# Kernel optimization log

Hardware: AMD Instinct MI355X
Metric: run time of the kernel (lower is better)

The kernel has to match this reference:

```python
import jax, jax.numpy as jnp
import numpy as np

N = 50000      # nodes
E = 800000     # edges (avg degree 16)
IN_DIM = 128
H = 4          # attention heads
D = 32         # hidden dim per head
NEG_SLOPE = 0.2


def setup_inputs() -> dict:
    key = jax.random.key(0)
    ks = jax.random.split(key, 9)
    x = jax.random.normal(ks[0], (N, IN_DIM), dtype=jnp.float32)
    src = jax.random.randint(ks[1], (E,), 0, N, dtype=jnp.int64)
    dst = jax.random.randint(ks[2], (E,), 0, N, dtype=jnp.int64)
    # layer 0: IN_DIM -> H*D ; layer 1: H*D -> H*D
    s0 = 1.0 / np.sqrt(IN_DIM)
    s1 = 1.0 / np.sqrt(H * D)
    W1 = jax.random.normal(ks[3], (H * D, IN_DIM), dtype=jnp.float32) * s0
    al1 = jax.random.normal(ks[4], (1, H, D), dtype=jnp.float32) * s1
    ar1 = jax.random.normal(ks[5], (1, H, D), dtype=jnp.float32) * s1
    W2 = jax.random.normal(ks[6], (H * D, H * D), dtype=jnp.float32) * s1
    al2 = jax.random.normal(ks[7], (1, H, D), dtype=jnp.float32) * s1
    ar2 = jax.random.normal(ks[8], (1, H, D), dtype=jnp.float32) * s1
    return {"x": x, "src": src, "dst": dst, "W1": W1, "al1": al1, "ar1": ar1,
            "W2": W2, "al2": al2, "ar2": ar2}


def gat_conv(h, src, dst, W, al, ar):
    """DGL-style GATConv. h: [N, F_in] -> [N, H, D], with ELU activation."""
    feat = (h @ W.T).reshape(N, H, D)                 # [N,H,D]
    el = jnp.sum(feat * al, axis=-1)                  # [N,H] a_l . Wh
    er = jnp.sum(feat * ar, axis=-1)                  # [N,H] a_r . Wh
    e = jax.nn.leaky_relu(el[src] + er[dst], NEG_SLOPE)  # [E,H]
    # numerically stable edge softmax over incoming edges of each dst node
    m = jax.ops.segment_max(e, dst, num_segments=N)   # [N,H]
    ee = jnp.exp(e - m[dst])                          # [E,H]
    denom = jax.ops.segment_sum(ee, dst, num_segments=N)  # [N,H]
    alpha = ee / denom[dst]                           # [E,H]
    msg = feat[src] * alpha[..., None]                # [E,H,D]
    out = jax.ops.segment_sum(msg, dst, num_segments=N)   # [N,H,D]
    return jax.nn.elu(out)


def reference(x, src, dst, W1, al1, ar1, W2, al2, ar2):
    h = gat_conv(x, src, dst, W1, al1, ar1).reshape(N, H * D)  # flatten(1)
    h = gat_conv(h, src, dst, W2, al2, ar2)                    # [N,H,D]
    return jnp.mean(h, axis=1)                                 # [N,D]
```

## Files before the change

### kernel.cpp

```cpp
#include <hip/hip_runtime.h>
#include <cmath>
#include <type_traits>

#define HEADS 4
#define FDIM 128
#define NEG 0.2f
#define NBUCK 8
#define CSHIFT 7
#define CMASK 127

typedef __attribute__((ext_vector_type(8))) __bf16 bf16x8;
typedef __attribute__((ext_vector_type(8))) _Float16 h16x8;
typedef __attribute__((ext_vector_type(4))) float f32x4;

__global__ __launch_bounds__(256) void prep_kernel(
    const float* __restrict__ W1, const float* __restrict__ al1,
    const float* __restrict__ ar1,
    const float* __restrict__ W2, const float* __restrict__ al2,
    const float* __restrict__ ar2,
    __bf16* __restrict__ wf1, __bf16* __restrict__ wext1,
    _Float16* __restrict__ wf2, _Float16* __restrict__ wext2)
{
    const int b = blockIdx.x, tid = threadIdx.x;
    if (b < 256) {
        int idx = (b & 127) * 256 + tid;
        int j = idx & 7;
        int r = idx >> 3;
        int c = r & 15; r >>= 4;
        int t = r & 7;  r >>= 3;
        int kq = r & 15;
        int hl = r >> 4;
        if (b < 128) {
            float v = W1[(t * 16 + c) * 128 + kq * 8 + j];
            __bf16 hi = (__bf16)v;
            wf1[idx] = (hl == 0) ? hi : (__bf16)(v - (float)hi);
        } else {
            float v = W2[(t * 16 + c) * 128 + kq * 8 + j];
            _Float16 hi = (_Float16)v;
            wf2[idx] = (hl == 0) ? hi : (_Float16)(v - (float)hi);
        }
    } else {
        const float* W  = (b == 256) ? W1 : W2;
        const float* al = (b == 256) ? al1 : al2;
        const float* ar = (b == 256) ? ar1 : ar2;
        __shared__ float val[1024];
        #pragma unroll
        for (int ch = 0; ch < 4; ++ch) {
            int idx = ch * 256 + tid;
            int c = idx >> 7, k = idx & 127;
            int h = c & 3;
            const float* a = (c < 4) ? al : ar;
            float s = 0.f;
            for (int d = 0; d < 32; ++d)
                s += a[h * 32 + d] * W[(h * 32 + d) * 128 + k];
            val[c * 128 + k] = s;
        }
        __syncthreads();
        #pragma unroll
        for (int ch = 0; ch < 16; ++ch) {
            int idx = tid * 16 + ch;
            int j = idx & 7;
            int r = idx >> 3;
            int c = r & 15; r >>= 4;
            int kq = r & 15;
            int hl = r >> 4;
            float v = (c < 8) ? val[c * 128 + kq * 8 + j] : 0.f;
            if (b == 256) {
                __bf16 hi = (__bf16)v;
                wext1[idx] = (hl == 0) ? hi : (__bf16)(v - (float)hi);
            } else {
                _Float16 hi = (_Float16)v;
                wext2[idx] = (hl == 0) ? hi : (_Float16)(v - (float)hi);
            }
        }
    }
}

__device__ __forceinline__ void gemm_body_f32(
    const float* __restrict__ X, const bf16x8* __restrict__ wf,
    const bf16x8* __restrict__ wext, _Float16* __restrict__ featH,
    float* __restrict__ el, float* __restrict__ er,
    int nnodes, int tile0, int tend, int stride, bf16x8* lw)
{
    const int tid = threadIdx.x;
    const int wave = tid >> 6, lane = tid & 63;
    const int l15 = lane & 15, quad = lane >> 4;

    int tile = tile0;
    float xr[32], xn[32];

    auto loadX = [&](int tl, float* dst) {
        int nodeA = tl * 64 + wave * 16 + l15;
        bool v = nodeA < nnodes;
        const float4* xp = (const float4*)(X + (size_t)nodeA * 128);
        #pragma unroll
        for (int ks = 0; ks < 4; ++ks) {
            float4 a = v ? xp[ks * 8 + quad * 2]     : make_float4(0.f, 0.f, 0.f, 0.f);
            float4 b = v ? xp[ks * 8 + quad * 2 + 1] : make_float4(0.f, 0.f, 0.f, 0.f);
            dst[ks * 8 + 0] = a.x; dst[ks * 8 + 1] = a.y;
            dst[ks * 8 + 2] = a.z; dst[ks * 8 + 3] = a.w;
            dst[ks * 8 + 4] = b.x; dst[ks * 8 + 5] = b.y;
            dst[ks * 8 + 6] = b.z; dst[ks * 8 + 7] = b.w;
        }
    };

    loadX(tile, xr);
    for (int i = tid; i < 2048; i += 256) lw[i] = wf[i];
    __syncthreads();

    while (true) {
        int next = tile + stride;
        if (next < tend) loadX(next, xn);

        f32x4 acc[9];
        #pragma unroll
        for (int t = 0; t < 9; ++t) acc[t] = (f32x4){0.f, 0.f, 0.f, 0.f};

        #pragma unroll
        for (int ks = 0; ks < 4; ++ks) {
            bf16x8 ahi, alo;
            #pragma unroll
            for (int j = 0; j < 8; ++j) {
                float xv = xr[ks * 8 + j];
                __bf16 h = (__bf16)xv;
                ahi[j] = h;
                alo[j] = (__bf16)(xv - (float)h);
            }
            const int kq = ks * 4 + quad;

            {
                bf16x8 bh = wext[(kq) * 16 + l15];
                bf16x8 bl = wext[(16 + kq) * 16 + l15];
                acc[8] = __builtin_amdgcn_mfma_f32_16x16x32_bf16(ahi, bh, acc[8], 0, 0, 0);
                acc[8] = __builtin_amdgcn_mfma_f32_16x16x32_bf16(alo, bh, acc[8], 0, 0, 0);
                acc[8] = __builtin_amdgcn_mfma_f32_16x16x32_bf16(ahi, bl, acc[8], 0, 0, 0);
            }
            #pragma unroll
            for (int t = 0; t < 8; ++t) {
                bf16x8 bh = lw[(kq * 8 + t) * 16 + l15];
                bf16x8 bl = wf[2048 + (kq * 8 + t) * 16 + l15];
                acc[t] = __builtin_amdgcn_mfma_f32_16x16x32_bf16(ahi, bh, acc[t], 0, 0, 0);
                acc[t] = __builtin_amdgcn_mfma_f32_16x16x32_bf16(alo, bh, acc[t], 0, 0, 0);
                acc[t] = __builtin_amdgcn_mfma_f32_16x16x32_bf16(ahi, bl, acc[t], 0, 0, 0);
            }
        }

        const int nodeC = tile * 64 + wave * 16 + quad * 4;
        #pragma unroll
        for (int r = 0; r < 4; ++r) {
            int gn = nodeC + r;
            if (gn < nnodes) {
                #pragma unroll
                for (int t = 0; t < 8; ++t)
                    featH[(size_t)gn * 128 + t * 16 + l15] = (_Float16)acc[t][r];
            }
        }
        if (l15 < 8) {
            #pragma unroll
            for (int r = 0; r < 4; ++r) {
                int gn = nodeC + r;
                if (gn < nnodes) {
                    if (l15 < 4) el[gn * HEADS + l15] = acc[8][r];
                    else         er[gn * HEADS + (l15 - 4)] = acc[8][r];
                }
            }
        }

        if (next >= tend) break;
        #pragma unroll
        for (int i = 0; i < 32; ++i) xr[i] = xn[i];
        tile = next;
    }
}

__device__ __forceinline__ void coarse_hist_body(
    const int* __restrict__ dst, int* __restrict__ histmat,
    int nedges, int nblk, int nbkt, int eb, int* chist)
{
    const int tid = threadIdx.x;
    for (int i = tid; i < nbkt; i += 256) chist[i] = 0;
    __syncthreads();
    int i0 = eb * 2048 + tid * 8;
    if (i0 + 7 < nedges) {
        int4 d0 = *(const int4*)&dst[i0];
        int4 d1 = *(const int4*)&dst[i0 + 4];
        atomicAdd(&chist[d0.x >> CSHIFT], 1);
        atomicAdd(&chist[d0.y >> CSHIFT], 1);
        atomicAdd(&chist[d0.z >> CSHIFT], 1);
        atomicAdd(&chist[d0.w >> CSHIFT], 1);
        atomicAdd(&chist[d1.x >> CSHIFT], 1);
        atomicAdd(&chist[d1.y >> CSHIFT], 1);
        atomicAdd(&chist[d1.z >> CSHIFT], 1);
        atomicAdd(&chist[d1.w >> CSHIFT], 1);
    } else {
        for (int i = i0; i < nedges; ++i)
            atomicAdd(&chist[dst[i] >> CSHIFT], 1);
    }
    __syncthreads();
    for (int i = tid; i < nbkt; i += 256)
        histmat[i * nblk + eb] = chist[i];
}

__device__ __forceinline__ void coarse_scatter_body(
    const int* __restrict__ src, const int* __restrict__ dst,
    const int* __restrict__ histoff, int* __restrict__ tmp,
    int nedges, int nblk, int nbkt, int eb, int* chist)
{
    const int tid = threadIdx.x;
    for (int i = tid; i < nbkt; i += 256) chist[i] = 0;
    __syncthreads();
    int i0 = eb * 2048 + tid * 8;
    if (i0 + 7 < nedges) {
        int s[8], d[8];
        *(int4*)&s[0] = *(const int4*)&src[i0];
        *(int4*)&s[4] = *(const int4*)&src[i0 + 4];
        *(int4*)&d[0] = *(const int4*)&dst[i0];
        *(int4*)&d[4] = *(const int4*)&dst[i0 + 4];
        #pragma unroll
        for (int q = 0; q < 8; ++q) {
            int bkt = d[q] >> CSHIFT;
            int r = atomicAdd(&chist[bkt], 1);
            int pos = histoff[bkt * nblk + eb] + r;
            tmp[pos] = ((d[q] & CMASK) << 16) | s[q];
        }
    } else {
        for (int i = i0; i < nedges; ++i) {
            int s = src[i], d = dst[i];
            int bkt = d >> CSHIFT;
            int r = atomicAdd(&chist[bkt], 1);
            tmp[histoff[bkt * nblk + eb] + r] = ((d & CMASK) << 16) | s;
        }
    }
}

__global__ __launch_bounds__(256) void fused_gemm_chist(
    const float* __restrict__ X, const bf16x8* __restrict__ wf,
    const bf16x8* __restrict__ wext, _Float16* __restrict__ featH,
    float* __restrict__ el, float* __restrict__ er, int nnodes,
    int t0, int tend, int gemm_blocks,
    const int* __restrict__ dst, int* __restrict__ histmat,
    int nedges, int nblk, int nbkt)
{
    __shared__ bf16x8 lw[2048];
    __shared__ int chist[512];
    if ((int)blockIdx.x < gemm_blocks)
        gemm_body_f32(X, wf, wext, featH, el, er, nnodes,
                      t0 + blockIdx.x, tend, gemm_blocks, lw);
    else
        coarse_hist_body(dst, histmat, nedges, nblk, nbkt,
                         blockIdx.x - gemm_blocks, chist);
}

__global__ __launch_bounds__(256) void fused_gemm_cscatter(
    const float* __restrict__ X, const bf16x8* __restrict__ wf,
    const bf16x8* __restrict__ wext, _Float16* __restrict__ featH,
    float* __restrict__ el, float* __restrict__ er, int nnodes,
    int t0, int tend, int gemm_blocks,
    const int* __restrict__ src, const int* __restrict__ dst,
    const int* __restrict__ histoff, int* __restrict__ tmp,
    int nedges, int nblk, int nbkt)
{
    __shared__ bf16x8 lw[2048];
    __shared__ int chist[512];
    if ((int)blockIdx.x < gemm_blocks)
        gemm_body_f32(X, wf, wext, featH, el, er, nnodes,
                      t0 + blockIdx.x, tend, gemm_blocks, lw);
    else
        coarse_scatter_body(src, dst, histoff, tmp, nedges, nblk, nbkt,
                            blockIdx.x - gemm_blocks, chist);
}

__global__ __launch_bounds__(256) void fine_sort_kernel(
    const int* __restrict__ tmp, const int* __restrict__ histoff,
    int* __restrict__ csr_src, int* __restrict__ offsets,
    int nblk, int nbkt, int nb, int nedges, int shift)
{
    __shared__ int eds[4096];
    __shared__ int fh[1024];
    __shared__ int wsums[4];
    const int b = blockIdx.x, tid = threadIdx.x;
    const int lane = tid & 63, w = tid >> 6;

    const int base = histoff[b * nblk];
    const int endb = histoff[(b + 1) * nblk];
    int cnt = endb - base;
    if (cnt > 4096) cnt = 4096;

    #pragma unroll
    for (int i = 0; i < 4; ++i) fh[tid + i * 256] = 0;
    __syncthreads();

    for (int i = tid; i < cnt; i += 256) {
        int e = tmp[base + i];
        eds[i] = e;
        int fb = ((e >> 16) << 3) + ((e & 0xffff) >> shift);
        atomicAdd(&fh[fb], 1);
    }
    __syncthreads();

    int v0 = fh[tid * 4], v1 = fh[tid * 4 + 1], v2 = fh[tid * 4 + 2], v3 = fh[tid * 4 + 3];
    int s0 = v0, s1 = s0 + v1, s2 = s1 + v2, s3 = s2 + v3;
    int x = s3;
    #pragma unroll
    for (int off = 1; off < 64; off <<= 1) {
        int t = __shfl_up(x, off, 64);
        if (lane >= off) x += t;
    }
    if (lane == 63) wsums[w] = x;
    __syncthreads();
    int wbase = 0;
    #pragma unroll
    for (int k = 0; k < 4; ++k) if (k < w) wbase += wsums[k];
    const int tb = wbase + x - s3;

    int o0 = tb, o1 = tb + s0, o2 = tb + s1, o3 = tb + s2;
    fh[tid * 4]     = o0;
    fh[tid * 4 + 1] = o1;
    fh[tid * 4 + 2] = o2;
    fh[tid * 4 + 3] = o3;
    int g = b * 1024 + tid * 4;
    if (g < nb)     offsets[g]     = base + o0;
    if (g + 1 < nb) offsets[g + 1] = base + o1;
    if (g + 2 < nb) offsets[g + 2] = base + o2;
    if (g + 3 < nb) offsets[g + 3] = base + o3;
    __syncthreads();

    for (int i = tid; i < cnt; i += 256) {
        int e = eds[i];
        int fb = ((e >> 16) << 3) + ((e & 0xffff) >> shift);
        int p = atomicAdd(&fh[fb], 1);
        csr_src[base + p] = e & 0xffff;
    }
    if (b == 0 && tid == 0) offsets[nb] = nedges;
}

__global__ __launch_bounds__(256) void scan1_kernel(
    const int* __restrict__ counts, int* __restrict__ offsets,
    int* __restrict__ bsums, int n)
{
    __shared__ int wsums[4];
    const int tid = threadIdx.x, lane = tid & 63, w = tid >> 6;
    const int i = blockIdx.x * 1024 + tid * 4;

    int4 v = make_int4(0, 0, 0, 0);
    if (i + 3 < n) v = *(const int4*)&counts[i];
    else {
        if (i < n)     v.x = counts[i];
        if (i + 1 < n) v.y = counts[i + 1];
        if (i + 2 < n) v.z = counts[i + 2];
    }
    int s0 = v.x, s1 = s0 + v.y, s2 = s1 + v.z, s3 = s2 + v.w;

    int x = s3;
    #pragma unroll
    for (int off = 1; off < 64; off <<= 1) {
        int t = __shfl_up(x, off, 64);
        if (lane >= off) x += t;
    }
    if (lane == 63) wsums[w] = x;
    __syncthreads();
    int wbase = 0;
    #pragma unroll
    for (int k = 0; k < 4; ++k) if (k < w) wbase += wsums[k];

    int tbase = wbase + x - s3;
    if (i < n)     offsets[i]     = tbase;
    if (i + 1 < n) offsets[i + 1] = tbase + s0;
    if (i + 2 < n) offsets[i + 2] = tbase + s1;
    if (i + 3 < n) offsets[i + 3] = tbase + s2;
    if (tid == 255) bsums[blockIdx.x] = wbase + x;
}

__global__ __launch_bounds__(256) void scan23_kernel(
    int* __restrict__ offsets, const int* __restrict__ bsums, int n, int nedges)
{
    __shared__ int sbase;
    const int tid = threadIdx.x, b = blockIdx.x;
    if (tid < 64) {
        int s = 0;
        for (int i = tid; i < b; i += 64) s += bsums[i];
        #pragma unroll
        for (int off = 1; off < 64; off <<= 1) s += __shfl_xor(s, off, 64);
        if (tid == 0) sbase = s;
    }
    __syncthreads();
    const int base = sbase;
    const int i = b * 1024 + tid * 4;
    #pragma unroll
    for (int k = 0; k < 4; ++k)
        if (i + k < n) offsets[i + k] += base;
    if (b == 0 && tid == 0) offsets[n] = nedges;
}

__device__ __forceinline__ void agg_one_node(
    const h16x8* __restrict__ frow, const float* __restrict__ el,
    const int* __restrict__ csr_src, int beg, int end,
    int g, int u, int h, float ern, float* r)
{
    float a[8];
    #pragma unroll
    for (int p = 0; p < 8; ++p) a[p] = 0.f;
    float sw = 0.f;
    const int iters = (end - beg + 3) >> 2;

    int ja = beg + g;
    int jb = ja + 4;
    int jc = ja + 8;
    int jd = ja + 12;
    bool va = ja < end, vb = jb < end;
    int sa = va ? csr_src[ja] : 0;
    int sb = vb ? csr_src[jb] : 0;
    int sc = jc < end ? csr_src[jc] : 0;
    int sd = jd < end ? csr_src[jd] : 0;
    float qa = el[sa * HEADS + h];
    float qb = el[sb * HEADS + h];
    h16x8 fa = frow[(size_t)sa * 16 + u];
    h16x8 fb = frow[(size_t)sb * 16 + u];

    for (int it = 0; it < iters; ++it) {
        int je = jd + 4;
        int se = je < end ? csr_src[je] : 0;
        float qc = el[sc * HEADS + h];
        h16x8 fc = frow[(size_t)sc * 16 + u];

        float e = qa + ern;
        e = e > 0.f ? e : NEG * e;
        float w2 = va ? __expf(e) : 0.f;
        #pragma unroll
        for (int p = 0; p < 8; ++p) a[p] += w2 * (float)fa[p];
        sw += w2;

        ja = jb; va = vb;
        jb = jc; vb = jb < end;
        qa = qb; fa = fb;
        qb = qc; fb = fc;
        sc = sd; sd = se;
        jc = jd; jd = je;
    }

    #pragma unroll
    for (int p = 0; p < 8; ++p) {
        a[p] += __shfl_xor(a[p], 16, 64);
        a[p] += __shfl_xor(a[p], 32, 64);
    }
    sw += __shfl_xor(sw, 16, 64);
    sw += __shfl_xor(sw, 32, 64);

    float inv = sw > 0.f ? 1.f / sw : 0.f;
    #pragma unroll
    for (int p = 0; p < 8; ++p) {
        float t = a[p] * inv;
        r[p] = t > 0.f ? t : __expf(t) - 1.f;
    }
}

__global__ __launch_bounds__(256) void fused_agg1_gemm2(
    const _Float16* __restrict__ featH, const float* __restrict__ el,
    const float* __restrict__ er, const int* __restrict__ offsets,
    const int* __restrict__ csr_src,
    const h16x8* __restrict__ wf, const h16x8* __restrict__ wext,
    _Float16* __restrict__ featH2, float* __restrict__ el2,
    float* __restrict__ er2, int nnodes)
{
    __shared__ h16x8 lw[2048];
    __shared__ h16x8 xt[1024];
    const int tid = threadIdx.x;
    const int wave = tid >> 6, lane = tid & 63;
    const int l15 = lane & 15, quad = lane >> 4;
    const int g = lane >> 4, u = lane & 15, h = u >> 2;
    const int tile = blockIdx.x;

    for (int i = tid; i < 2048; i += 256) lw[i] = wf[i];

    const h16x8* frow = (const h16x8*)featH;

    for (int i = 0; i < 16; ++i) {
        int row = wave * 16 + i;
        int n = tile * 64 + row;
        int scol = u ^ (row & 15);
        if (n < nnodes) {
            int beg = offsets[n * NBUCK], end = offsets[n * NBUCK + NBUCK];
            float ern = er[n * HEADS + h];
            float r[8];
            agg_one_node(frow, el, csr_src, beg, end, g, u, h, ern, r);
            if (g == 0) {
                h16x8 o;
                #pragma unroll
                for (int p = 0; p < 8; ++p) o[p] = (_Float16)r[p];
                xt[row * 16 + scol] = o;
            }
        } else if (g == 0) {
            h16x8 z;
            #pragma unroll
            for (int p = 0; p < 8; ++p) z[p] = (_Float16)0.f;
            xt[row * 16 + scol] = z;
        }
    }
    __syncthreads();

    f32x4 acc[9];
    #pragma unroll
    for (int t = 0; t < 9; ++t) acc[t] = (f32x4){0.f, 0.f, 0.f, 0.f};

    #pragma unroll
    for (int ks = 0; ks < 4; ++ks) {
        const int kq = ks * 4 + quad;
        h16x8 a = xt[(wave * 16 + l15) * 16 + (kq ^ l15)];
        {
            h16x8 bh = wext[(kq) * 16 + l15];
            h16x8 bl = wext[(16 + kq) * 16 + l15];
            acc[8] = __builtin_amdgcn_mfma_f32_16x16x32_f16(a, bh, acc[8], 0, 0, 0);
            acc[8] = __builtin_amdgcn_mfma_f32_16x16x32_f16(a, bl, acc[8], 0, 0, 0);
        }
        #pragma unroll
        for (int t = 0; t < 8; ++t) {
            h16x8 bh = lw[(kq * 8 + t) * 16 + l15];
            h16x8 bl = wf[2048 + (kq * 8 + t) * 16 + l15];
            acc[t] = __builtin_amdgcn_mfma_f32_16x16x32_f16(a, bh, acc[t], 0, 0, 0);
            acc[t] = __builtin_amdgcn_mfma_f32_16x16x32_f16(a, bl, acc[t], 0, 0, 0);
        }
    }

    const int nodeC = tile * 64 + wave * 16 + quad * 4;
    #pragma unroll
    for (int r = 0; r < 4; ++r) {
        int gn = nodeC + r;
        if (gn < nnodes) {
            #pragma unroll
            for (int t = 0; t < 8; ++t)
                featH2[(size_t)gn * 128 + t * 16 + l15] = (_Float16)acc[t][r];
        }
    }
    if (l15 < 8) {
        #pragma unroll
        for (int r = 0; r < 4; ++r) {
            int gn = nodeC + r;
            if (gn < nnodes) {
                if (l15 < 4) el2[gn * HEADS + l15] = acc[8][r];
                else         er2[gn * HEADS + (l15 - 4)] = acc[8][r];
            }
        }
    }
}

__global__ __launch_bounds__(256) void aggregate_mean_kernel(
    const _Float16* __restrict__ featH, const float* __restrict__ el,
    const float* __restrict__ er, const int* __restrict__ offsets,
    const int* __restrict__ csr_src, float* __restrict__ outp, int nnodes)
{
    const int n = (blockIdx.x * 256 + threadIdx.x) >> 6;
    if (n >= nnodes) return;
    const int lane = threadIdx.x & 63;
    const int g = lane >> 4, u = lane & 15, h = u >> 2;
    const int beg = offsets[n * NBUCK], end = offsets[n * NBUCK + NBUCK];
    const float ern = er[n * HEADS + h];

    float r[8];
    agg_one_node((const h16x8*)featH, el, csr_src, beg, end, g, u, h, ern, r);

    #pragma unroll
    for (int p = 0; p < 8; ++p) {
        r[p] += __shfl_xor(r[p], 4, 64);
        r[p] += __shfl_xor(r[p], 8, 64);
    }
    if (g == 0 && u < 4) {
        float4* o4 = (float4*)(outp + (size_t)n * 32 + u * 8);
        o4[0] = make_float4(0.25f * r[0], 0.25f * r[1], 0.25f * r[2], 0.25f * r[3]);
        o4[1] = make_float4(0.25f * r[4], 0.25f * r[5], 0.25f * r[6], 0.25f * r[7]);
    }
}

extern "C" void kernel_launch(void* const* d_in, const int* in_sizes, int n_in,
                              void* d_out, int out_size, void* d_ws, size_t ws_size,
                              hipStream_t stream)
{
    const float* x   = (const float*)d_in[0];
    const int*   src = (const int*)d_in[1];
    const int*   dst = (const int*)d_in[2];
    const float* W1  = (const float*)d_in[3];
    const float* al1 = (const float*)d_in[4];
    const float* ar1 = (const float*)d_in[5];
    const float* W2  = (const float*)d_in[6];
    const float* al2 = (const float*)d_in[7];
    const float* ar2 = (const float*)d_in[8];

    const int N = in_sizes[0] / FDIM;
    const int E = in_sizes[1];
    const int NB = N * NBUCK;

    int shift = 0;
    while (((N - 1) >> shift) > (NBUCK - 1)) ++shift;

    const int NBKT  = (N + CMASK) >> CSHIFT;
    const int NBLK1 = (E + 2047) >> 11;
    const int n1    = NBKT * NBLK1;

    _Float16* featH  = (_Float16*)d_ws;
    _Float16* featH2 = featH + (size_t)N * FDIM;
    float* el1 = (float*)(featH2 + (size_t)N * FDIM);
    float* er1 = el1 + (size_t)N * HEADS;
    float* el2 = er1 + (size_t)N * HEADS;
    float* er2 = el2 + (size_t)N * HEADS;
    uintptr_t tp = ((uintptr_t)(er2 + (size_t)N * HEADS) + 15) & ~(uintptr_t)15;
    int* tmp     = (int*)tp;
    int* histmat = tmp + E;
    int* histoff = histmat + n1;
    int* offsets = histoff + (n1 + 1);
    int* csr_src = offsets + (NB + 1);
    int* bsums   = csr_src + E;
    uintptr_t wp = ((uintptr_t)(bsums + 512) + 63) & ~(uintptr_t)63;
    __bf16* wf1     = (__bf16*)wp;
    __bf16* wext1   = wf1 + 32768;
    _Float16* wf2   = (_Float16*)(wext1 + 4096);
    _Float16* wext2 = wf2 + 32768;

    const int ntiles = (N + 63) / 64;
    const int halfT  = (ntiles + 1) / 2;
    const int gA = halfT < 256 ? halfT : 256;
    const int gB = (ntiles - halfT) < 256 ? (ntiles - halfT) : 256;
    const int agg_grid  = (N + 3) / 4;
    const int nscan     = (n1 + 1023) / 1024;

    prep_kernel<<<258, 256, 0, stream>>>(
        W1, al1, ar1, W2, al2, ar2, wf1, wext1, wf2, wext2);

    fused_gemm_chist<<<gA + NBLK1, 256, 0, stream>>>(
        x, (const bf16x8*)wf1, (const bf16x8*)wext1, featH, el1, er1, N,
        0, halfT, gA, dst, histmat, E, NBLK1, NBKT);

    scan1_kernel<<<nscan, 256, 0, stream>>>(histmat, histoff, bsums, n1);
    scan23_kernel<<<nscan, 256, 0, stream>>>(histoff, bsums, n1, E);

    fused_gemm_cscatter<<<gB + NBLK1, 256, 0, stream>>>(
        x, (const bf16x8*)wf1, (const bf16x8*)wext1, featH, el1, er1, N,
        halfT, ntiles, gB, src, dst, histoff, tmp, E, NBLK1, NBKT);

    fine_sort_kernel<<<NBKT, 256, 0, stream>>>(
        tmp, histoff, csr_src, offsets, NBLK1, NBKT, NB, E, shift);

    fused_agg1_gemm2<<<ntiles, 256, 0, stream>>>(
        featH, el1, er1, offsets, csr_src,
        (const h16x8*)wf2, (const h16x8*)wext2, featH2, el2, er2, N);

    aggregate_mean_kernel<<<agg_grid, 256, 0, stream>>>(
        featH2, el2, er2, offsets, csr_src, (float*)d_out, N);
}
```

Measured before the change: 257.0 us.

## Split layer-1 aggregation from GEMM2 and overlap halves across launches

New measurement: 217.8 us. 1.18x faster.

```diff
diff --git a/kernel.cpp b/kernel.cpp
--- a/kernel.cpp
+++ b/kernel.cpp
@@ -173,6 +173,76 @@
     }
 }
 
+__device__ __forceinline__ void gemm2_tile(
+    const _Float16* __restrict__ X, const h16x8* __restrict__ wf,
+    const h16x8* __restrict__ wext, _Float16* __restrict__ featH2,
+    float* __restrict__ el2, float* __restrict__ er2, int nnodes, int tile)
+{
+    const int tid = threadIdx.x;
+    const int wave = tid >> 6, lane = tid & 63;
+    const int l15 = lane & 15, quad = lane >> 4;
+
+    h16x8 xr[4];
+    {
+        int nodeA = tile * 64 + wave * 16 + l15;
+        bool v = nodeA < nnodes;
+        const h16x8* xp = (const h16x8*)(X + (size_t)nodeA * 128);
+        #pragma unroll
+        for (int ks = 0; ks < 4; ++ks) {
+            if (v) {
+                xr[ks] = xp[ks * 4 + quad];
+            } else {
+                #pragma unroll
+                for (int j = 0; j < 8; ++j) xr[ks][j] = (_Float16)0.f;
+            }
+        }
+    }
+
+    f32x4 acc[9];
+    #pragma unroll
+    for (int t = 0; t < 9; ++t) acc[t] = (f32x4){0.f, 0.f, 0.f, 0.f};
+
+    #pragma unroll
+    for (int ks = 0; ks < 4; ++ks) {
+        h16x8 a = xr[ks];
+        const int kq = ks * 4 + quad;
+        {
+            h16x8 bh = wext[(kq) * 16 + l15];
+            h16x8 bl = wext[(16 + kq) * 16 + l15];
+            acc[8] = __builtin_amdgcn_mfma_f32_16x16x32_f16(a, bh, acc[8], 0, 0, 0);
+            acc[8] = __builtin_amdgcn_mfma_f32_16x16x32_f16(a, bl, acc[8], 0, 0, 0);
+        }
+        #pragma unroll
+        for (int t = 0; t < 8; ++t) {
+            h16x8 bh = wf[(kq * 8 + t) * 16 + l15];
+            h16x8 bl = wf[2048 + (kq * 8 + t) * 16 + l15];
+            acc[t] = __builtin_amdgcn_mfma_f32_16x16x32_f16(a, bh, acc[t], 0, 0, 0);
+            acc[t] = __builtin_amdgcn_mfma_f32_16x16x32_f16(a, bl, acc[t], 0, 0, 0);
+        }
+    }
+
+    const int nodeC = tile * 64 + wave * 16 + quad * 4;
+    #pragma unroll
+    for (int r = 0; r < 4; ++r) {
+        int gn = nodeC + r;
+        if (gn < nnodes) {
+            #pragma unroll
+            for (int t = 0; t < 8; ++t)
+                featH2[(size_t)gn * 128 + t * 16 + l15] = (_Float16)acc[t][r];
+        }
+    }
+    if (l15 < 8) {
+        #pragma unroll
+        for (int r = 0; r < 4; ++r) {
+            int gn = nodeC + r;
+            if (gn < nnodes) {
+                if (l15 < 4) el2[gn * HEADS + l15] = acc[8][r];
+                else         er2[gn * HEADS + (l15 - 4)] = acc[8][r];
+            }
+        }
+    }
+}
+
 __device__ __forceinline__ void coarse_hist_body(
     const int* __restrict__ dst, int* __restrict__ histmat,
     int nedges, int nblk, int nbkt, int eb, int* chist)
@@ -454,120 +524,82 @@
     }
 }
 
-__global__ __launch_bounds__(256) void fused_agg1_gemm2(
+template <bool MEAN>
+__global__ __launch_bounds__(256, 8) void aggregate_kernel(
     const _Float16* __restrict__ featH, const float* __restrict__ el,
     const float* __restrict__ er, const int* __restrict__ offsets,
-    const int* __restrict__ csr_src,
-    const h16x8* __restrict__ wf, const h16x8* __restrict__ wext,
+    const int* __restrict__ csr_src, void* __restrict__ outp,
+    int n0, int nend)
+{
+    const int n = n0 + ((blockIdx.x * 256 + threadIdx.x) >> 6);
+    if (n >= nend) return;
+    const int lane = threadIdx.x & 63;
+    const int g = lane >> 4, u = lane & 15, h = u >> 2;
+    const int beg = offsets[n * NBUCK], end = offsets[n * NBUCK + NBUCK];
+    const float ern = er[n * HEADS + h];
+
+    float r[8];
+    agg_one_node((const h16x8*)featH, el, csr_src, beg, end, g, u, h, ern, r);
+
+    if (!MEAN) {
+        if (g == 0) {
+            h16x8 o;
+            #pragma unroll
+            for (int p = 0; p < 8; ++p) o[p] = (_Float16)r[p];
+            ((h16x8*)outp)[(size_t)n * 16 + u] = o;
+        }
+    } else {
+        #pragma unroll
+        for (int p = 0; p < 8; ++p) {
+            r[p] += __shfl_xor(r[p], 4, 64);
+            r[p] += __shfl_xor(r[p], 8, 64);
+        }
+        if (g == 0 && u < 4) {
+            float* out = (float*)outp;
+            float4* o4 = (float4*)(out + (size_t)n * 32 + u * 8);
+            o4[0] = make_float4(0.25f * r[0], 0.25f * r[1], 0.25f * r[2], 0.25f * r[3]);
+            o4[1] = make_float4(0.25f * r[4], 0.25f * r[5], 0.25f * r[6], 0.25f * r[7]);
+        }
+    }
+}
+
+__global__ __launch_bounds__(256) void fused_agg_gemm2(
+    const _Float16* __restrict__ featH, const float* __restrict__ el1,
+    const float* __restrict__ er1, const int* __restrict__ offsets,
+    const int* __restrict__ csr_src, _Float16* __restrict__ h1,
+    const h16x8* __restrict__ wf2, const h16x8* __restrict__ wext2,
     _Float16* __restrict__ featH2, float* __restrict__ el2,
-    float* __restrict__ er2, int nnodes)
-{
-    __shared__ h16x8 lw[2048];
-    __shared__ h16x8 xt[1024];
-    const int tid = threadIdx.x;
-    const int wave = tid >> 6, lane = tid & 63;
-    const int l15 = lane & 15, quad = lane >> 4;
-    const int g = lane >> 4, u = lane & 15, h = u >> 2;
-    const int tile = blockIdx.x;
-
-    for (int i = tid; i < 2048; i += 256) lw[i] = wf[i];
-
-    const h16x8* frow = (const h16x8*)featH;
-
-    for (int i = 0; i < 16; ++i) {
-        int row = wave * 16 + i;
-        int n = tile * 64 + row;
-        int scol = u ^ (row & 15);
-        if (n < nnodes) {
-            int beg = offsets[n * NBUCK], end = offsets[n * NBUCK + NBUCK];
-            float ern = er[n * HEADS + h];
-            float r[8];
-            agg_one_node(frow, el, csr_src, beg, end, g, u, h, ern, r);
-            if (g == 0) {
-                h16x8 o;
-                #pragma unroll
-                for (int p = 0; p < 8; ++p) o[p] = (_Float16)r[p];
-                xt[row * 16 + scol] = o;
-            }
-        } else if (g == 0) {
-            h16x8 z;
-            #pragma unroll
-            for (int p = 0; p < 8; ++p) z[p] = (_Float16)0.f;
-            xt[row * 16 + scol] = z;
-        }
-    }
-    __syncthreads();
-
-    f32x4 acc[9];
-    #pragma unroll
-    for (int t = 0; t < 9; ++t) acc[t] = (f32x4){0.f, 0.f, 0.f, 0.f};
-
-    #pragma unroll
-    for (int ks = 0; ks < 4; ++ks) {
-        const int kq = ks * 4 + quad;
-        h16x8 a = xt[(wave * 16 + l15) * 16 + (kq ^ l15)];
-        {
-            h16x8 bh = wext[(kq) * 16 + l15];
-            h16x8 bl = wext[(16 + kq) * 16 + l15];
-            acc[8] = __builtin_amdgcn_mfma_f32_16x16x32_f16(a, bh, acc[8], 0, 0, 0);
-            acc[8] = __builtin_amdgcn_mfma_f32_16x16x32_f16(a, bl, acc[8], 0, 0, 0);
-        }
-        #pragma unroll
-        for (int t = 0; t < 8; ++t) {
-            h16x8 bh = lw[(kq * 8 + t) * 16 + l15];
-            h16x8 bl = wf[2048 + (kq * 8 + t) * 16 + l15];
-            acc[t] = __builtin_amdgcn_mfma_f32_16x16x32_f16(a, bh, acc[t], 0, 0, 0);
-            acc[t] = __builtin_amdgcn_mfma_f32_16x16x32_f16(a, bl, acc[t], 0, 0, 0);
-        }
-    }
-
-    const int nodeC = tile * 64 + wave * 16 + quad * 4;
-    #pragma unroll
-    for (int r = 0; r < 4; ++r) {
-        int gn = nodeC + r;
-        if (gn < nnodes) {
-            #pragma unroll
-            for (int t = 0; t < 8; ++t)
-                featH2[(size_t)gn * 128 + t * 16 + l15] = (_Float16)acc[t][r];
-        }
-    }
-    if (l15 < 8) {
-        #pragma unroll
-        for (int r = 0; r < 4; ++r) {
-            int gn = nodeC + r;
-            if (gn < nnodes) {
-                if (l15 < 4) el2[gn * HEADS + l15] = acc[8][r];
-                else         er2[gn * HEADS + (l15 - 4)] = acc[8][r];
-            }
-        }
-    }
-}
-
-__global__ __launch_bounds__(256) void aggregate_mean_kernel(
-    const _Float16* __restrict__ featH, const float* __restrict__ el,
-    const float* __restrict__ er, const int* __restrict__ offsets,
-    const int* __restrict__ csr_src, float* __restrict__ outp, int nnodes)
-{
-    const int n = (blockIdx.x * 256 + threadIdx.x) >> 6;
+    float* __restrict__ er2, int n0, int nnodes, int gemmB)
+{
+    const int b = blockIdx.x;
+    if (b < gemmB) {
+        gemm2_tile(h1, wf2, wext2, featH2, el2, er2, nnodes, b);
+        return;
+    }
+    const int n = n0 + (((b - gemmB) * 256 + threadIdx.x) >> 6);
     if (n >= nnodes) return;
     const int lane = threadIdx.x & 63;
     const int g = lane >> 4, u = lane & 15, h = u >> 2;
     const int beg = offsets[n * NBUCK], end = offsets[n * NBUCK + NBUCK];
-    const float ern = er[n * HEADS + h];
+    const float ern = er1[n * HEADS + h];
 
     float r[8];
-    agg_one_node((const h16x8*)featH, el, csr_src, beg, end, g, u, h, ern, r);
-
-    #pragma unroll
-    for (int p = 0; p < 8; ++p) {
-        r[p] += __shfl_xor(r[p], 4, 64);
-        r[p] += __shfl_xor(r[p], 8, 64);
-    }
-    if (g == 0 && u < 4) {
-        float4* o4 = (float4*)(outp + (size_t)n * 32 + u * 8);
-        o4[0] = make_float4(0.25f * r[0], 0.25f * r[1], 0.25f * r[2], 0.25f * r[3]);
-        o4[1] = make_float4(0.25f * r[4], 0.25f * r[5], 0.25f * r[6], 0.25f * r[7]);
-    }
+    agg_one_node((const h16x8*)featH, el1, csr_src, beg, end, g, u, h, ern, r);
+
+    if (g == 0) {
+        h16x8 o;
+        #pragma unroll
+        for (int p = 0; p < 8; ++p) o[p] = (_Float16)r[p];
+        ((h16x8*)h1)[(size_t)n * 16 + u] = o;
+    }
+}
+
+__global__ __launch_bounds__(256) void gemm2_half_kernel(
+    const _Float16* __restrict__ h1, const h16x8* __restrict__ wf2,
+    const h16x8* __restrict__ wext2, _Float16* __restrict__ featH2,
+    float* __restrict__ el2, float* __restrict__ er2, int nnodes, int t0)
+{
+    gemm2_tile(h1, wf2, wext2, featH2, el2, er2, nnodes, t0 + blockIdx.x);
 }
 
 extern "C" void kernel_launch(void* const* d_in, const int* in_sizes, int n_in,
@@ -595,7 +627,8 @@
     const int NBLK1 = (E + 2047) >> 11;
     const int n1    = NBKT * NBLK1;
 
-    _Float16* featH  = (_Float16*)d_ws;
+    _Float16* h1     = (_Float16*)d_ws;
+    _Float16* featH  = h1 + (size_t)N * FDIM;
     _Float16* featH2 = featH + (size_t)N * FDIM;
     float* el1 = (float*)(featH2 + (size_t)N * FDIM);
     float* er1 = el1 + (size_t)N * HEADS;
@@ -618,8 +651,13 @@
     const int halfT  = (ntiles + 1) / 2;
     const int gA = halfT < 256 ? halfT : 256;
     const int gB = (ntiles - halfT) < 256 ? (ntiles - halfT) : 256;
-    const int agg_grid  = (N + 3) / 4;
-    const int nscan     = (n1 + 1023) / 1024;
+    const int nscan  = (n1 + 1023) / 1024;
+
+    const int halfT2 = ntiles / 2;
+    const int halfN  = halfT2 * 64;
+    const int agg1A_blocks = (halfN + 3) / 4;
+    const int agg1B_blocks = (N - halfN + 3) / 4;
+    const int agg2_blocks  = (N + 3) / 4;
 
     prep_kernel<<<258, 256, 0, stream>>>(
         W1, al1, ar1, W2, al2, ar2, wf1, wext1, wf2, wext2);
@@ -638,10 +676,17 @@
     fine_sort_kernel<<<NBKT, 256, 0, stream>>>(
         tmp, histoff, csr_src, offsets, NBLK1, NBKT, NB, E, shift);
 
-    fused_agg1_gemm2<<<ntiles, 256, 0, stream>>>(
-        featH, el1, er1, offsets, csr_src,
-        (const h16x8*)wf2, (const h16x8*)wext2, featH2, el2, er2, N);
-
-    aggregate_mean_kernel<<<agg_grid, 256, 0, stream>>>(
-        featH2, el2, er2, offsets, csr_src, (float*)d_out, N);
-}
+    aggregate_kernel<false><<<agg1A_blocks, 256, 0, stream>>>(
+        featH, el1, er1, offsets, csr_src, (void*)h1, 0, halfN);
+
+    fused_agg_gemm2<<<halfT2 + agg1B_blocks, 256, 0, stream>>>(
+        featH, el1, er1, offsets, csr_src, h1,
+        (const h16x8*)wf2, (const h16x8*)wext2, featH2, el2, er2,
+        halfN, N, halfT2);
+
+    gemm2_half_kernel<<<ntiles - halfT2, 256, 0, stream>>>(
+        h1, (const h16x8*)wf2, (const h16x8*)wext2, featH2, el2, er2, N, halfT2);
+
+    aggregate_kernel<true><<<agg2_blocks, 256, 0, stream>>>(
+        featH2, el2, er2, offsets, csr_src, d_out, 0, N);
+}
```
